# Kernel tuning notes

Measured on AMD Instinct MI355X. Metric: run time of the kernel, lower is better.

## Reference

```python
import jax, jax.numpy as jnp
import numpy as np

# Dimensions (match init_kwargs / input_specs)
B, C, H, W = 16, 96, 224, 224
COUT = 96
PH, PW = 16, 16          # patch_size (== patch_stride, non-overlapping)
KH, KW = 3, 3            # patch_kernel and output_kernel
PAD = 1                  # padding
GH, GW = H // PH, W // PW
P = GH * GW              # num_patches = 196


def setup_inputs() -> dict:
    key = jax.random.key(0)
    k1, k2, k3 = jax.random.split(key, 3)
    x = jax.random.normal(k1, (B, C, H, W), dtype=jnp.float32)
    # kaiming-normal-ish init scales (fan_in over trailing dims, as torch does)
    pf = jax.random.normal(k2, (C, P, 1, KH, KW), dtype=jnp.float32) * np.float32(np.sqrt(2.0 / (P * KH * KW)))
    of = jax.random.normal(k3, (COUT, C, KH, KW), dtype=jnp.float32) * np.float32(np.sqrt(2.0 / (C * KH * KW)))
    return {"x": x, "patch_filters": pf, "output_filters": of}


def _self_conv2d(x, patch_filters):
    """Locally-connected per-patch depthwise conv.

    x: (B, C, H, W); patch_filters: (C, P, 1, KH, KW).
    Each of the P non-overlapping PHxPW patches of each channel is convolved
    with its own KHxKW kernel (padding=PAD, stride=1), then patches are
    reassembled into the full (B, C, H, W) map.
    """
    # (B, C, GH, PH, GW, PW) -> (B, C, GH, GW, PH, PW) -> (B, C*P, PH, PW)
    xp = x.reshape(B, C, GH, PH, GW, PW).transpose(0, 1, 2, 4, 3, 5).reshape(B, C * P, PH, PW)
    k = patch_filters.reshape(C * P, 1, KH, KW)
    y = jax.lax.conv_general_dilated(
        xp, k,
        window_strides=(1, 1),
        padding=[(PAD, PAD), (PAD, PAD)],
        feature_group_count=C * P,
        dimension_numbers=("NCHW", "OIHW", "NCHW"),
    )  # (B, C*P, PH, PW) since 3x3 conv with pad 1 preserves size
    return y.reshape(B, C, GH, GW, PH, PW).transpose(0, 1, 2, 4, 3, 5).reshape(B, C, H, W)


def reference(x, patch_filters, output_filters):
    # input already at (max_input_height, max_input_width) -> F.pad is a no-op
    sa = _self_conv2d(x, patch_filters)
    out = jax.lax.conv_general_dilated(
        sa, output_filters,
        window_strides=(1, 1),
        padding=[(PAD, PAD), (PAD, PAD)],
        dimension_numbers=("NCHW", "OIHW", "NCHW"),
    )  # (B, COUT, H, W)
    return jax.nn.gelu(out, approximate=False)  # torch nn.GELU() = exact erf gelu
```

## Files before the change

kernel.cpp:

```cpp
#include <hip/hip_runtime.h>
#include <hip/hip_bf16.h>

#define B_    16
#define C_    96
#define H_    224
#define W_    224
#define COUT_ 96
#define GH_   14
#define GW_   14
#define P_    196
#define HW_   (H_*W_)
#define NCH_  12
#define APITCH 181

#define AS1 __attribute__((address_space(1)))
#define AS3 __attribute__((address_space(3)))

typedef __attribute__((ext_vector_type(8))) unsigned short ushort8;
typedef __attribute__((ext_vector_type(8))) short        short8;
typedef __attribute__((ext_vector_type(4))) float        f32x4;

__device__ __forceinline__ unsigned short f2bf(float f) {
    union { __hip_bfloat16 h; unsigned short u; } cv;
    cv.h = __float2bfloat16(f);
    return cv.u;
}

__global__ __launch_bounds__(256) void sa_prep_kernel(const float* __restrict__ x,
                                                      const float* __restrict__ pf,
                                                      unsigned short* __restrict__ sa,
                                                      const float* __restrict__ of,
                                                      unsigned short* __restrict__ ofb3,
                                                      unsigned short* __restrict__ zp) {
    int bid = blockIdx.x;

    if (bid >= B_ * P_) {
        int pb = bid - B_ * P_;
        if (pb == 0 && threadIdx.x < 128) zp[threadIdx.x] = 0;
        int e = pb * 256 + threadIdx.x;
        if (e < 82944) {
            int j    = e & 7;
            int l    = (e >> 3) & 63;
            int ni   = (e >> 9) % 6;
            int cs   = (e / 3072) % 3;
            int tap  = e / 9216;
            int cout = ni * 16 + (l & 15);
            int c    = cs * 32 + (l >> 4) * 8 + j;
            ofb3[e] = f2bf(of[((size_t)cout * 96 + c) * 9 + tap]);
        }
        return;
    }

    int patch = bid % P_;
    int b     = bid / P_;
    int gh = patch / GW_, gw = patch % GW_;
    int t  = threadIdx.x;
    int py = t >> 4, px = t & 15;
    int y  = gh * 16 + py, xx = gw * 16 + px;

    __shared__ float xs[2][8][256];

    const float* xp0 = x + (size_t)b * C_ * HW_ + (size_t)y * W_ + xx;

    float lf[8];
    #pragma unroll
    for (int ch = 0; ch < 8; ++ch) lf[ch] = xp0[(size_t)ch * HW_];

    for (int cc = 0; cc < NCH_; ++cc) {
        int buf = cc & 1;
        #pragma unroll
        for (int ch = 0; ch < 8; ++ch) xs[buf][ch][t] = lf[ch];
        __syncthreads();
        if (cc < NCH_ - 1) {
            #pragma unroll
            for (int ch = 0; ch < 8; ++ch)
                lf[ch] = xp0[(size_t)((cc + 1) * 8 + ch) * HW_];
        }

        ushort8 v;
        #pragma unroll
        for (int ch = 0; ch < 8; ++ch) {
            const float* wgt = pf + ((size_t)(cc * 8 + ch) * P_ + patch) * 9;
            float a = 0.f;
            #pragma unroll
            for (int dy = -1; dy <= 1; ++dy) {
                int yy = py + dy;
                if ((unsigned)yy < 16u) {
                    #pragma unroll
                    for (int dx = -1; dx <= 1; ++dx) {
                        int xq = px + dx;
                        if ((unsigned)xq < 16u)
                            a = fmaf(xs[buf][ch][yy * 16 + xq],
                                     wgt[(dy + 1) * 3 + (dx + 1)], a);
                    }
                }
            }
            v[ch] = f2bf(a);
        }
        *(ushort8*)&sa[(((size_t)(b * NCH_ + cc) * H_ + y) * W_ + xx) * 8] = v;
    }
}

__global__ __launch_bounds__(256, 3) void conv2_mfma(const unsigned short* __restrict__ sa,
                                                     const unsigned short* __restrict__ ofb3,
                                                     const unsigned short* __restrict__ zp,
                                                     float* __restrict__ out) {
    int bid0 = blockIdx.x;
    int bid  = (bid0 % 8) * (6272 / 8) + bid0 / 8;
    int half = bid & 1;
    int pid  = bid >> 1;
    int patch = pid % P_;
    int b     = pid / P_;
    int gh = patch / GW_, gw = patch % GW_;
    int y0 = gh * 16 + half * 8, x0 = gw * 16;

    int t = threadIdx.x;
    int w = t >> 6, l = t & 63;
    int wm = w & 1, wn = w >> 1;
    int mrow = l & 15, kgrp = l >> 4;

    __shared__ ushort8 at8[2304];

    #pragma unroll
    for (int i = 0; i < 9; ++i) {
        int v = t + i * 256;
        const unsigned short* src = zp;
        if (v < 2172) {
            int ccl = v / APITCH, hpx = v - ccl * APITCH;
            if (hpx < 180) {
                int gy = y0 - 1 + hpx / 18, gx = x0 - 1 + hpx % 18;
                if ((unsigned)gy < (unsigned)H_ && (unsigned)gx < (unsigned)W_)
                    src = &sa[(((size_t)(b * NCH_ + ccl) * H_ + gy) * W_ + gx) * 8];
            }
        }
        __builtin_amdgcn_global_load_lds((const AS1 unsigned int*)src,
                                         (AS3 unsigned int*)&at8[v], 16, 0, 0);
    }

    f32x4 acc[4][3];
    #pragma unroll
    for (int mi = 0; mi < 4; ++mi)
        #pragma unroll
        for (int ni = 0; ni < 3; ++ni)
            acc[mi][ni] = (f32x4)0.f;

    __syncthreads();

    const unsigned short* at = (const unsigned short*)at8;

    short8 bfA[3], bfB[3], afA[4], afB[4];
    auto LOADBF = [&](short8* dst, int T) {
        const unsigned short* p = ofb3 + (size_t)(T / 3) * 9216 + (T % 3) * 3072
                                  + (wn * 3) * 512 + l * 8;
        #pragma unroll
        for (int nj = 0; nj < 3; ++nj)
            dst[nj] = *(const short8*)&p[nj * 512];
    };
    auto LOADAF = [&](short8* dst, int T) {
        int tap = T / 3, cs = T % 3;
        int ky = tap / 3, kx = tap % 3;
        #pragma unroll
        for (int mi = 0; mi < 4; ++mi)
            dst[mi] = *(const short8*)&at[((cs * 4 + kgrp) * APITCH
                                          + (wm * 4 + mi + ky) * 18
                                          + kx + mrow) * 8];
    };

    LOADBF(bfA, 0);
    LOADAF(afA, 0);
    #pragma unroll
    for (int T = 0; T < 27; ++T) {
        short8* bcur = (T & 1) ? bfB : bfA;
        short8* bnxt = (T & 1) ? bfA : bfB;
        short8* acur = (T & 1) ? afB : afA;
        short8* anxt = (T & 1) ? afA : afB;
        if (T + 1 < 27) {
            LOADBF(bnxt, T + 1);
            LOADAF(anxt, T + 1);
        }
        __builtin_amdgcn_sched_barrier(0);

        #pragma unroll
        for (int mi = 0; mi < 4; ++mi)
            #pragma unroll
            for (int nj = 0; nj < 3; ++nj)
                acc[mi][nj] = __builtin_amdgcn_mfma_f32_16x16x32_bf16(
                    acur[mi], bcur[nj], acc[mi][nj], 0, 0, 0);
    }

    #pragma unroll
    for (int mi = 0; mi < 4; ++mi) {
        int gy = y0 + wm * 4 + mi;
        #pragma unroll
        for (int nj = 0; nj < 3; ++nj) {
            int cout = (wn * 3 + nj) * 16 + mrow;
            f32x4 gv;
            #pragma unroll
            for (int j = 0; j < 4; ++j) {
                float vv = acc[mi][nj][j];
                gv[j] = 0.5f * vv * (1.0f + erff(vv * 0.70710678118f));
            }
            *(f32x4*)&out[((size_t)b * COUT_ + cout) * HW_ + (size_t)gy * W_ +
                          x0 + kgrp * 4] = gv;
        }
    }
}

extern "C" void kernel_launch(void* const* d_in, const int* in_sizes, int n_in,
                              void* d_out, int out_size, void* d_ws, size_t ws_size,
                              hipStream_t stream) {
    const float* x  = (const float*)d_in[0];
    const float* pf = (const float*)d_in[1];
    const float* of = (const float*)d_in[2];
    float* out = (float*)d_out;

    unsigned short* sa   = (unsigned short*)d_ws;
    unsigned short* ofb3 = (unsigned short*)((char*)d_ws + 154140672);
    unsigned short* zp   = (unsigned short*)((char*)d_ws + 154306560);

    sa_prep_kernel<<<B_ * P_ + 324, 256, 0, stream>>>(x, pf, sa, of, ofb3, zp);
    conv2_mfma<<<B_ * P_ * 2, 256, 0, stream>>>(sa, ofb3, zp, out);
}
```

Measured before the change: 363.0 us.

## Switch conv2 to 32x32x16 MFMA with full-patch tiles per block

The output conv now uses 32x32x16 bf16 MFMA instead of 16x16x32. Each block computes a whole 16x16 patch (256 pixels x 96 couts) rather than half a patch, so the halo overhead shrinks and the MFMA count drops. The filter prepack layout is reordered to match the new B-operand fragment. Risks: LDS rises to 64KB per block and occupancy falls to 2 blocks. The epilogue writes 16 scalar floats per accumulator instead of 4-wide vector stores, which may hurt output write coalescing.

```diff
diff --git a/kernel.cpp b/kernel.cpp
--- a/kernel.cpp
+++ b/kernel.cpp
@@ -11,14 +11,15 @@
 #define P_    196
 #define HW_   (H_*W_)
 #define NCH_  12
-#define APITCH 181
+#define APITCH 325
 
 #define AS1 __attribute__((address_space(1)))
 #define AS3 __attribute__((address_space(3)))
 
-typedef __attribute__((ext_vector_type(8))) unsigned short ushort8;
-typedef __attribute__((ext_vector_type(8))) short        short8;
-typedef __attribute__((ext_vector_type(4))) float        f32x4;
+typedef __attribute__((ext_vector_type(8)))  unsigned short ushort8;
+typedef __attribute__((ext_vector_type(8)))  short          short8;
+typedef __attribute__((ext_vector_type(4)))  float          f32x4;
+typedef __attribute__((ext_vector_type(16))) float          f32x16;
 
 __device__ __forceinline__ unsigned short f2bf(float f) {
     union { __hip_bfloat16 h; unsigned short u; } cv;
@@ -30,7 +31,7 @@
                                                       const float* __restrict__ pf,
                                                       unsigned short* __restrict__ sa,
                                                       const float* __restrict__ of,
-                                                      unsigned short* __restrict__ ofb3,
+                                                      unsigned short* __restrict__ ofb4,
                                                       unsigned short* __restrict__ zp) {
     int bid = blockIdx.x;
 
@@ -39,14 +40,14 @@
         if (pb == 0 && threadIdx.x < 128) zp[threadIdx.x] = 0;
         int e = pb * 256 + threadIdx.x;
         if (e < 82944) {
-            int j    = e & 7;
-            int l    = (e >> 3) & 63;
-            int ni   = (e >> 9) % 6;
-            int cs   = (e / 3072) % 3;
-            int tap  = e / 9216;
-            int cout = ni * 16 + (l & 15);
-            int c    = cs * 32 + (l >> 4) * 8 + j;
-            ofb3[e] = f2bf(of[((size_t)cout * 96 + c) * 9 + tap]);
+            int j   = e & 7;
+            int l   = (e >> 3) & 63;
+            int nt  = (e >> 9) % 3;
+            int q   = (e / 1536) % 6;
+            int tap = e / 9216;
+            int cout = nt * 32 + (l & 31);
+            int c    = q * 16 + (l >> 5) * 8 + j;
+            ofb4[e] = f2bf(of[((size_t)cout * 96 + c) * 9 + tap]);
         }
         return;
     }
@@ -101,33 +102,30 @@
     }
 }
 
-__global__ __launch_bounds__(256, 3) void conv2_mfma(const unsigned short* __restrict__ sa,
-                                                     const unsigned short* __restrict__ ofb3,
+__global__ __launch_bounds__(256, 2) void conv2_mfma(const unsigned short* __restrict__ sa,
+                                                     const unsigned short* __restrict__ ofb4,
                                                      const unsigned short* __restrict__ zp,
                                                      float* __restrict__ out) {
     int bid0 = blockIdx.x;
-    int bid  = (bid0 % 8) * (6272 / 8) + bid0 / 8;
-    int half = bid & 1;
-    int pid  = bid >> 1;
-    int patch = pid % P_;
-    int b     = pid / P_;
+    int bid  = (bid0 % 8) * (3136 / 8) + bid0 / 8;
+    int patch = bid % P_;
+    int b     = bid / P_;
     int gh = patch / GW_, gw = patch % GW_;
-    int y0 = gh * 16 + half * 8, x0 = gw * 16;
+    int y0 = gh * 16, x0 = gw * 16;
 
     int t = threadIdx.x;
     int w = t >> 6, l = t & 63;
-    int wm = w & 1, wn = w >> 1;
-    int mrow = l & 15, kgrp = l >> 4;
-
-    __shared__ ushort8 at8[2304];
-
-    #pragma unroll
-    for (int i = 0; i < 9; ++i) {
+    int hi = l >> 5;
+
+    __shared__ ushort8 at8[4096];
+
+    #pragma unroll
+    for (int i = 0; i < 16; ++i) {
         int v = t + i * 256;
         const unsigned short* src = zp;
-        if (v < 2172) {
+        if (v < 3900) {
             int ccl = v / APITCH, hpx = v - ccl * APITCH;
-            if (hpx < 180) {
+            if (hpx < 324) {
                 int gy = y0 - 1 + hpx / 18, gx = x0 - 1 + hpx % 18;
                 if ((unsigned)gy < (unsigned)H_ && (unsigned)gx < (unsigned)W_)
                     src = &sa[(((size_t)(b * NCH_ + ccl) * H_ + gy) * W_ + gx) * 8];
@@ -137,33 +135,37 @@
                                          (AS3 unsigned int*)&at8[v], 16, 0, 0);
     }
 
-    f32x4 acc[4][3];
-    #pragma unroll
-    for (int mi = 0; mi < 4; ++mi)
-        #pragma unroll
-        for (int ni = 0; ni < 3; ++ni)
-            acc[mi][ni] = (f32x4)0.f;
+    f32x16 acc[2][3];
+    #pragma unroll
+    for (int mt = 0; mt < 2; ++mt)
+        #pragma unroll
+        for (int nt = 0; nt < 3; ++nt)
+            acc[mt][nt] = (f32x16)0.f;
 
     __syncthreads();
 
     const unsigned short* at = (const unsigned short*)at8;
 
-    short8 bfA[3], bfB[3], afA[4], afB[4];
+    short8 bfA[6], bfB[6], afA[4], afB[4];
     auto LOADBF = [&](short8* dst, int T) {
-        const unsigned short* p = ofb3 + (size_t)(T / 3) * 9216 + (T % 3) * 3072
-                                  + (wn * 3) * 512 + l * 8;
-        #pragma unroll
-        for (int nj = 0; nj < 3; ++nj)
-            dst[nj] = *(const short8*)&p[nj * 512];
+        const unsigned short* p = ofb4 + (size_t)(T / 3) * 9216 + (T % 3) * 3072 + l * 8;
+        #pragma unroll
+        for (int d = 0; d < 6; ++d)
+            dst[d] = *(const short8*)&p[d * 512];
     };
     auto LOADAF = [&](short8* dst, int T) {
         int tap = T / 3, cs = T % 3;
         int ky = tap / 3, kx = tap % 3;
-        #pragma unroll
-        for (int mi = 0; mi < 4; ++mi)
-            dst[mi] = *(const short8*)&at[((cs * 4 + kgrp) * APITCH
-                                          + (wm * 4 + mi + ky) * 18
-                                          + kx + mrow) * 8];
+        int hx = (l & 15) + kx;
+        int yb = 4 * w + ((l >> 4) & 1);
+        #pragma unroll
+        for (int mt = 0; mt < 2; ++mt)
+            #pragma unroll
+            for (int qi = 0; qi < 2; ++qi) {
+                int plane = 4 * cs + 2 * qi + hi;
+                int hy = yb + 2 * mt + ky;
+                dst[mt * 2 + qi] = *(const short8*)&at[(plane * APITCH + hy * 18 + hx) * 8];
+            }
     };
 
     LOADBF(bfA, 0);
@@ -181,27 +183,29 @@
         __builtin_amdgcn_sched_barrier(0);
 
         #pragma unroll
-        for (int mi = 0; mi < 4; ++mi)
-            #pragma unroll
-            for (int nj = 0; nj < 3; ++nj)
-                acc[mi][nj] = __builtin_amdgcn_mfma_f32_16x16x32_bf16(
-                    acur[mi], bcur[nj], acc[mi][nj], 0, 0, 0);
-    }
-
-    #pragma unroll
-    for (int mi = 0; mi < 4; ++mi) {
-        int gy = y0 + wm * 4 + mi;
-        #pragma unroll
-        for (int nj = 0; nj < 3; ++nj) {
-            int cout = (wn * 3 + nj) * 16 + mrow;
-            f32x4 gv;
-            #pragma unroll
-            for (int j = 0; j < 4; ++j) {
-                float vv = acc[mi][nj][j];
-                gv[j] = 0.5f * vv * (1.0f + erff(vv * 0.70710678118f));
-            }
-            *(f32x4*)&out[((size_t)b * COUT_ + cout) * HW_ + (size_t)gy * W_ +
-                          x0 + kgrp * 4] = gv;
+        for (int mt = 0; mt < 2; ++mt)
+            #pragma unroll
+            for (int nt = 0; nt < 3; ++nt)
+                #pragma unroll
+                for (int qi = 0; qi < 2; ++qi)
+                    acc[mt][nt] = __builtin_amdgcn_mfma_f32_32x32x16_bf16(
+                        acur[mt * 2 + qi], bcur[qi * 3 + nt], acc[mt][nt], 0, 0, 0);
+    }
+
+    #pragma unroll
+    for (int mt = 0; mt < 2; ++mt) {
+        #pragma unroll
+        for (int nt = 0; nt < 3; ++nt) {
+            int cout = nt * 32 + (l & 31);
+            float* ob = out + ((size_t)b * COUT_ + cout) * HW_;
+            #pragma unroll
+            for (int r = 0; r < 16; ++r) {
+                int m  = (r & 3) + 8 * (r >> 2) + 4 * hi;
+                int px = w * 64 + mt * 32 + m;
+                int gy = y0 + (px >> 4), gx = x0 + (px & 15);
+                float vv = acc[mt][nt][r];
+                ob[(size_t)gy * W_ + gx] = 0.5f * vv * (1.0f + erff(vv * 0.70710678118f));
+            }
         }
     }
 }
@@ -215,9 +219,9 @@
     float* out = (float*)d_out;
 
     unsigned short* sa   = (unsigned short*)d_ws;
-    unsigned short* ofb3 = (unsigned short*)((char*)d_ws + 154140672);
+    unsigned short* ofb4 = (unsigned short*)((char*)d_ws + 154140672);
     unsigned short* zp   = (unsigned short*)((char*)d_ws + 154306560);
 
-    sa_prep_kernel<<<B_ * P_ + 324, 256, 0, stream>>>(x, pf, sa, of, ofb3, zp);
-    conv2_mfma<<<B_ * P_ * 2, 256, 0, stream>>>(sa, ofb3, zp, out);
-}
+    sa_prep_kernel<<<B_ * P_ + 324, 256, 0, stream>>>(x, pf, sa, of, ofb4, zp);
+    conv2_mfma<<<B_ * P_, 256, 0, stream>>>(sa, ofb4, zp, out);
+}
```

Measured after the change: 458.5 us. 1.26x slower.
